# Kernel optimization log

Hardware: AMD Instinct MI355X
Metric: run time of the kernel (lower is better)

## Reference

```python
import jax, jax.numpy as jnp
import numpy as np

STRIDE = 2
IN_CH = 64
F_SCALE = 2
EMBED = 64  # int(in_ch * ss_exp_factor)


def _pixel_unshuffle(x, f):
    # out[b, (fi*f+fj)*c + cc, h, w] = x[b, cc, h*f+fi, w*f+fj]
    b, c, H, W = x.shape
    x = x.reshape(b, c, H // f, f, W // f, f)
    x = x.transpose(0, 3, 5, 1, 2, 4)  # b, fi, fj, c, h, w
    return x.reshape(b, f * f * c, H // f, W // f)


def _pixel_shuffle(x, f):
    b, fc, h, w = x.shape
    c = fc // (f * f)
    x = x.reshape(b, f, f, c, h, w)
    x = x.transpose(0, 3, 4, 1, 5, 2)  # b, c, h, fi, w, fj
    return x.reshape(b, c, h * f, w * f)


def _conv(x, w, b, dilation):
    out = jax.lax.conv_general_dilated(
        x, w, window_strides=(1, 1),
        padding=[(dilation, dilation), (dilation, dilation)],
        rhs_dilation=(dilation, dilation),
        dimension_numbers=('NCHW', 'OIHW', 'NCHW'))
    return out + b[None, :, None, None]


def _conv1x1(x, w, b):
    out = jax.lax.conv_general_dilated(
        x, w, window_strides=(1, 1), padding=[(0, 0), (0, 0)],
        dimension_numbers=('NCHW', 'OIHW', 'NCHW'))
    return out + b[None, :, None, None]


def _attention(x, wqk, f):
    b, c, H, W = x.shape
    # layer_norm over (c,h,w), no affine
    mu = jnp.mean(x, axis=(1, 2, 3), keepdims=True)
    var = jnp.var(x, axis=(1, 2, 3), keepdims=True)
    xx = (x - mu) / jnp.sqrt(var + 1e-5)
    ph, pw = (f - H % f) % f, (f - W % f) % f
    if ph or pw:
        xx = jnp.pad(xx, ((0, 0), (0, 0), (0, ph), (0, pw)))
        xv = jnp.pad(x, ((0, 0), (0, 0), (0, ph), (0, pw)))
    else:
        xv = x
    sh, sw = (H + ph) // f, (W + pw) // f
    B = b * f * f
    xu = _pixel_unshuffle(xx, f).reshape(B, c, sh, sw)
    vu = _pixel_unshuffle(xv, f).reshape(B, c, sh, sw)
    n = sh * sw
    qk = xu.transpose(0, 2, 3, 1).reshape(B, n, c)  # (B, n, c)
    v = vu.transpose(0, 2, 3, 1).reshape(B, n, c)
    q = qk @ wqk  # (B, n, e)
    q = q / jnp.maximum(jnp.linalg.norm(q, axis=-1, keepdims=True), 1e-12)
    attn = jnp.einsum('bne,bme->bnm', q, q) / jnp.sqrt(jnp.float32(wqk.shape[1]))
    attn = jax.nn.softmax(attn, axis=-1)
    out = jnp.einsum('bnm,bmc->bnc', attn, v)  # (B, n, c)
    out = out.reshape(B, sh, sw, c).transpose(0, 3, 1, 2)
    out = out.reshape(b, f * f * c, sh, sw)
    out = _pixel_shuffle(out, f)
    return out[:, :, :H, :W]


def setup_inputs() -> dict:
    key = jax.random.key(0)
    ks = jax.random.split(key, 8)
    c = IN_CH
    s3 = 1.0 / np.sqrt(c * 9)
    s1 = 1.0 / np.sqrt(c)
    return {
        'x': jax.random.normal(ks[0], (8, c, 128, 128), dtype=jnp.float32),
        'wqk': jax.random.normal(ks[1], (c, EMBED), dtype=jnp.float32) * np.sqrt(6.0 / (c + EMBED)),
        'conv1_w': jax.random.normal(ks[2], (c, c, 3, 3), dtype=jnp.float32) * s3,
        'conv1_b': jnp.zeros((c,), dtype=jnp.float32),
        'conv2_w': jax.random.normal(ks[3], (c, c, 3, 3), dtype=jnp.float32) * s3,
        'conv2_b': jnp.zeros((c,), dtype=jnp.float32),
        'conv3_w': jax.random.normal(ks[4], (c, c, 1, 1), dtype=jnp.float32) * s1,
        'conv3_b': jnp.zeros((c,), dtype=jnp.float32),
    }


def reference(x, wqk, conv1_w, conv1_b, conv2_w, conv2_b, conv3_w, conv3_b):
    f = F_SCALE * STRIDE
    a = x + _attention(x, wqk, f)
    y = jax.nn.relu(_conv(a, conv1_w, conv1_b, STRIDE))
    y = jax.nn.relu(_conv(y, conv2_w, conv2_b, STRIDE))
    y = _conv1x1(y, conv3_w, conv3_b)
    return x + y
```

## Files before the change

### kernel.cpp

```cpp
#include <hip/hip_runtime.h>

typedef unsigned short u16;
typedef unsigned int   u32;

typedef __attribute__((ext_vector_type(8))) short s16x8;
typedef __attribute__((ext_vector_type(4))) float f32x4;

__device__ __forceinline__ float bf2f(u16 u){
  union { u32 i; float f; } v; v.i = ((u32)u) << 16; return v.f;
}
__device__ __forceinline__ u16 f2bf(float f){
  union { float f; u32 i; } v; v.f = f;
  u32 x = v.i;
  return (u16)((x + 0x7fffu + ((x >> 16) & 1u)) >> 16);
}


__global__ __launch_bounds__(256) void k_lnstats(const float* __restrict__ x, float* __restrict__ stats){
  const int bb    = blockIdx.x >> 7;
  const int chunk = blockIdx.x & 127;
  const float4* p = (const float4*)(x + bb*1048576 + chunk*8192);
  float s = 0.f, ss = 0.f;
  #pragma unroll
  for (int i=0;i<8;++i){
    float4 v = p[threadIdx.x + (i<<8)];
    s  += v.x + v.y + v.z + v.w;
    ss += v.x*v.x + v.y*v.y + v.z*v.z + v.w*v.w;
  }
  #pragma unroll
  for (int off=32; off; off>>=1){ s += __shfl_down(s, off); ss += __shfl_down(ss, off); }
  __shared__ float rs[4], rss[4];
  const int lane = threadIdx.x & 63, wv = threadIdx.x >> 6;
  if (lane == 0){ rs[wv] = s; rss[wv] = ss; }
  __syncthreads();
  if (threadIdx.x == 0){
    atomicAdd(&stats[bb*2+0], rs[0]+rs[1]+rs[2]+rs[3]);
    atomicAdd(&stats[bb*2+1], rss[0]+rss[1]+rss[2]+rss[3]);
  }
}

__global__ __launch_bounds__(256) void k_wt(const float* __restrict__ w, u16* __restrict__ wt){
  int e = blockIdx.x*256 + threadIdx.x;
  int tap = e >> 12, co = (e >> 6) & 63, ci = e & 63;
  wt[e] = f2bf(w[(co*64 + ci)*9 + tap]);
}

__global__ __launch_bounds__(256) void k_qv(const float* __restrict__ x, const float* __restrict__ wqk,
                                            const float* __restrict__ stats,
                                            u16* __restrict__ qb, u16* __restrict__ vb){
  const int Bb = blockIdx.x >> 4;
  const int mt = blockIdx.x & 15;
  const int b = Bb >> 4, fi = (Bb >> 2) & 3, fj = Bb & 3;
  const float inv_n = 1.f/1048576.f;
  const float mu   = stats[2*b] * inv_n;
  const float var  = stats[2*b+1]*inv_n - mu*mu;
  const float rstd = rsqrtf(var + 1e-5f);

  __shared__ float xt[64][68];
  __shared__ float wk[64][68];
  __shared__ float red[64][17];
  const int t = threadIdx.x;
  const int m0 = mt << 6;

  #pragma unroll
  for (int i=0;i<16;++i){ int e = t+(i<<8); wk[e>>6][e&63] = wqk[e]; }
  #pragma unroll
  for (int i=0;i<16;++i){
    int e = t+(i<<8); int cc = e>>6, ml = e&63;
    int m = m0 + ml;
    int hh = ((m>>5)<<2)+fi, ww = ((m&31)<<2)+fj;
    xt[ml][cc] = (x[(((b<<6)+cc)<<14)+(hh<<7)+ww] - mu)*rstd;
  }
  __syncthreads();

  const int ty = t>>4, tx = t&15;
  float acc[4][4] = {};
  for (int cc=0; cc<64; ++cc){
    float a0=xt[(ty<<2)+0][cc], a1=xt[(ty<<2)+1][cc], a2=xt[(ty<<2)+2][cc], a3=xt[(ty<<2)+3][cc];
    float b0=wk[cc][(tx<<2)+0], b1=wk[cc][(tx<<2)+1], b2=wk[cc][(tx<<2)+2], b3=wk[cc][(tx<<2)+3];
    acc[0][0]+=a0*b0; acc[0][1]+=a0*b1; acc[0][2]+=a0*b2; acc[0][3]+=a0*b3;
    acc[1][0]+=a1*b0; acc[1][1]+=a1*b1; acc[1][2]+=a1*b2; acc[1][3]+=a1*b3;
    acc[2][0]+=a2*b0; acc[2][1]+=a2*b1; acc[2][2]+=a2*b2; acc[2][3]+=a2*b3;
    acc[3][0]+=a3*b0; acc[3][1]+=a3*b1; acc[3][2]+=a3*b2; acc[3][3]+=a3*b3;
  }
  #pragma unroll
  for (int i=0;i<4;++i){
    float pn = acc[i][0]*acc[i][0]+acc[i][1]*acc[i][1]+acc[i][2]*acc[i][2]+acc[i][3]*acc[i][3];
    red[(ty<<2)+i][tx] = pn;
  }
  __syncthreads();
  float inv[4];
  #pragma unroll
  for (int i=0;i<4;++i){
    float s = 0.f;
    #pragma unroll
    for (int k=0;k<16;++k) s += red[(ty<<2)+i][k];
    inv[i] = 1.f / fmaxf(sqrtf(s), 1e-12f);
  }
  #pragma unroll
  for (int i=0;i<4;++i)
    #pragma unroll
    for (int j=0;j<4;++j)
      xt[(ty<<2)+i][(tx<<2)+j] = acc[i][j]*inv[i];
  __syncthreads();
  #pragma unroll
  for (int i=0;i<16;++i){
    int e = t+(i<<8); int ml = e>>6, ee = e&63;
    qb[((Bb<<10)+m0+ml)*64 + ee] = f2bf(xt[ml][ee]);
  }
  #pragma unroll
  for (int i=0;i<16;++i){
    int e = t+(i<<8); int cc = e>>6, ml = e&63;
    int m = m0 + ml;
    int hh = ((m>>5)<<2)+fi, ww = ((m&31)<<2)+fj;
    wk[ml][cc] = x[(((b<<6)+cc)<<14)+(hh<<7)+ww];
  }
  __syncthreads();
  #pragma unroll
  for (int i=0;i<16;++i){
    int e = t+(i<<8); int cc = e>>6, ml = e&63;
    vb[(Bb<<16) + (cc<<10) + m0 + ml] = f2bf(wk[ml][cc]);
  }
}

__global__ __launch_bounds__(256) void k_attn(const u16* __restrict__ qb, const u16* __restrict__ vb,
                                              const float* __restrict__ x, u16* __restrict__ apad){
  const int Bb = blockIdx.x >> 4;
  const int qt = blockIdx.x & 15;
  const int b = Bb>>4, fi=(Bb>>2)&3, fj=Bb&3;
  __shared__ __align__(16) char lds[24576];
  const int KS = 0, VS = 8192, PS = 16384;

  const int t = threadIdx.x;
  const int w = t >> 6, lane = t & 63;
  const int lrow = lane & 15, lk = lane >> 4;

  const u16* qB = qb + (Bb<<16);
  const u16* vB = vb + (Bb<<16);

  const u16* qrp = qB + ((qt<<6) + (w<<4) + lrow)*64;
  const s16x8 qf0 = *(const s16x8*)(qrp + (lk<<3));
  const s16x8 qf1 = *(const s16x8*)(qrp + 32 + (lk<<3));

  f32x4 o_acc[4] = {};
  float lp[4] = {0.f,0.f,0.f,0.f};

  for (int kt=0; kt<16; ++kt){
    __syncthreads();
    #pragma unroll
    for (int c = t; c < 512; c += 256){
      int row = c >> 3, slot = c & 7;
      uint4 kv = *(const uint4*)(qB + ((kt<<6)+row)*64 + (slot<<3));
      *(uint4*)(lds + KS + row*128 + (((slot ^ (row&7)))<<4)) = kv;
      uint4 vv = *(const uint4*)(vB + (row<<10) + (kt<<6) + (slot<<3));
      *(uint4*)(lds + VS + row*128 + (((slot ^ (row&7)))<<4)) = vv;
    }
    __syncthreads();

    f32x4 s_acc[4] = {};
    #pragma unroll
    for (int nt=0; nt<4; ++nt){
      int key = (nt<<4) + lrow;
      const char* kb = lds + KS + key*128;
      s16x8 kf0 = *(const s16x8*)(kb + ((lk       ^ (key&7))<<4));
      s16x8 kf1 = *(const s16x8*)(kb + (((4+lk)   ^ (key&7))<<4));
      s_acc[nt] = __builtin_amdgcn_mfma_f32_16x16x32_bf16(qf0, kf0, s_acc[nt], 0,0,0);
      s_acc[nt] = __builtin_amdgcn_mfma_f32_16x16x32_bf16(qf1, kf1, s_acc[nt], 0,0,0);
    }

    #pragma unroll
    for (int nt=0; nt<4; ++nt)
      #pragma unroll
      for (int r=0; r<4; ++r){
        float p = __expf(s_acc[nt][r]*0.125f);
        lp[r] += p;
        int prow = (w<<4) + (lk<<2) + r;
        int key  = (nt<<4) + lrow;
        *(u16*)(lds + PS + prow*128 + ((key<<1) ^ ((prow&7)<<4))) = f2bf(p);
      }

    {
      int prow = (w<<4) + lrow;
      const char* pb = lds + PS + prow*128;
      s16x8 pf0 = *(const s16x8*)(pb + ((lk     ^ (prow&7))<<4));
      s16x8 pf1 = *(const s16x8*)(pb + (((4+lk) ^ (prow&7))<<4));
      #pragma unroll
      for (int nt=0; nt<4; ++nt){
        int ch = (nt<<4) + lrow;
        const char* vbp = lds + VS + ch*128;
        s16x8 vf0 = *(const s16x8*)(vbp + ((lk     ^ (ch&7))<<4));
        s16x8 vf1 = *(const s16x8*)(vbp + (((4+lk) ^ (ch&7))<<4));
        o_acc[nt] = __builtin_amdgcn_mfma_f32_16x16x32_bf16(pf0, vf0, o_acc[nt], 0,0,0);
        o_acc[nt] = __builtin_amdgcn_mfma_f32_16x16x32_bf16(pf1, vf1, o_acc[nt], 0,0,0);
      }
    }
  }

  #pragma unroll
  for (int r=0;r<4;++r){
    float s = lp[r];
    s += __shfl_xor(s, 1); s += __shfl_xor(s, 2);
    s += __shfl_xor(s, 4); s += __shfl_xor(s, 8);
    lp[r] = 1.f / s;
  }

  __syncthreads();
  float* os = (float*)lds;
  #pragma unroll
  for (int nt=0; nt<4; ++nt)
    #pragma unroll
    for (int r=0; r<4; ++r)
      os[((w<<4)+(lk<<2)+r)*68 + (nt<<4)+lrow] = o_acc[nt][r]*lp[r];
  __syncthreads();

  const int m0 = qt << 6;
  #pragma unroll
  for (int i=0;i<16;++i){
    int e = t+(i<<8);
    int cc = e>>6, ml = e&63;
    int m = m0 + ml;
    int hh = ((m>>5)<<2)+fi, ww = ((m&31)<<2)+fj;
    os[ml*68 + cc] += x[(((b<<6)+cc)<<14) + (hh<<7) + ww];
  }
  __syncthreads();
  #pragma unroll
  for (int i=0;i<16;++i){
    int e = t+(i<<8);
    int ml = e>>6, cc = e&63;
    int m = m0 + ml;
    int hh = ((m>>5)<<2)+fi, ww = ((m&31)<<2)+fj;
    apad[((b*132 + hh+2)*132 + ww+2)*64 + cc] = f2bf(os[ml*68 + cc]);
  }
}

__global__ __launch_bounds__(256) void k_conv3m(const u16* __restrict__ in, const u16* __restrict__ wt,
                                                const float* __restrict__ bias, u16* __restrict__ outp){
  const int seg = blockIdx.x;
  const int h   = blockIdx.y;
  const int b   = blockIdx.z;
  const int t = threadIdx.x;
  const int wv = t >> 6, lane = t & 63;
  const int lrow = lane & 15, lk = lane >> 4;
  const int co0 = wv << 4;
  const int w0 = seg << 6;

  s16x8 A[9][2];
  #pragma unroll
  for (int tap=0; tap<9; ++tap)
    #pragma unroll
    for (int hf=0; hf<2; ++hf)
      A[tap][hf] = *(const s16x8*)(wt + (((tap<<6) + co0 + lrow)<<6) + (hf<<5) + (lk<<3));

  float4 b4 = *(const float4*)&bias[co0 + (lk<<2)];
  f32x4 binit = {b4.x, b4.y, b4.z, b4.w};
  f32x4 acc[4] = {binit, binit, binit, binit};

  const int base_b = b * (132*132);
  #pragma unroll
  for (int dh=0; dh<3; ++dh){
    const u16* rowp = in + ((base_b + (h + (dh<<1))*132)<<6);
    #pragma unroll
    for (int dw=0; dw<3; ++dw){
      #pragma unroll
      for (int hf=0; hf<2; ++hf){
        #pragma unroll
        for (int pt=0; pt<4; ++pt){
          int wp = w0 + (pt<<4) + lrow + (dw<<1);
          s16x8 B = *(const s16x8*)(rowp + (wp<<6) + (hf<<5) + (lk<<3));
          acc[pt] = __builtin_amdgcn_mfma_f32_16x16x32_bf16(A[dh*3+dw][hf], B, acc[pt], 0,0,0);
        }
      }
    }
  }

  #pragma unroll
  for (int pt=0; pt<4; ++pt){
    int wp = w0 + (pt<<4) + lrow + 2;
    u16* op = outp + ((base_b + (h+2)*132 + wp)<<6) + co0 + (lk<<2);
    ushort4 o4;
    o4.x = f2bf(fmaxf(acc[pt][0], 0.f));
    o4.y = f2bf(fmaxf(acc[pt][1], 0.f));
    o4.z = f2bf(fmaxf(acc[pt][2], 0.f));
    o4.w = f2bf(fmaxf(acc[pt][3], 0.f));
    *(ushort4*)op = o4;
  }
}

__global__ __launch_bounds__(256) void k_conv1x1(const u16* __restrict__ y2, const float* __restrict__ w3,
                                                 const float* __restrict__ b3, const float* __restrict__ x,
                                                 float* __restrict__ out){
  const int b  = blockIdx.x >> 6;
  const int p0 = (blockIdx.x & 63) << 8;
  __shared__ u16  ys[256][68];
  __shared__ float w3s[64][68];
  __shared__ float bs[64];
  const int t = threadIdx.x;
  #pragma unroll
  for (int i=0;i<16;++i){ int e = t+(i<<8); w3s[e & 63][e >> 6] = w3[e]; }
  if (t < 64) bs[t] = b3[t];
  #pragma unroll
  for (int i=0;i<64;++i){
    int e = t + (i<<8);
    int px = e >> 6, ci = e & 63;
    int pg = p0 + px; int hh = pg >> 7, ww = pg & 127;
    ys[px][ci] = y2[((b*132 + hh+2)*132 + ww+2)*64 + ci];
  }
  __syncthreads();
  const int cog = (t >> 6) << 4;
  const int pl  = t & 63;
  float acc[16][4];
  #pragma unroll
  for (int c=0;c<16;++c){
    float bvv = bs[cog+c];
    acc[c][0]=bvv; acc[c][1]=bvv; acc[c][2]=bvv; acc[c][3]=bvv;
  }
  for (int c4=0;c4<64;c4+=4){
    float yv[4][4];
    #pragma unroll
    for (int p=0;p<4;++p){
      ushort4 u = *(const ushort4*)&ys[pl + (p<<6)][c4];
      yv[p][0]=bf2f(u.x); yv[p][1]=bf2f(u.y); yv[p][2]=bf2f(u.z); yv[p][3]=bf2f(u.w);
    }
    #pragma unroll
    for (int cq=0;cq<4;++cq){
      float4 w0 = *(const float4*)&w3s[c4+0][cog+(cq<<2)];
      float4 w1 = *(const float4*)&w3s[c4+1][cog+(cq<<2)];
      float4 w2 = *(const float4*)&w3s[c4+2][cog+(cq<<2)];
      float4 w3v = *(const float4*)&w3s[c4+3][cog+(cq<<2)];
      #pragma unroll
      for (int p=0;p<4;++p){
        acc[(cq<<2)+0][p] += yv[p][0]*w0.x + yv[p][1]*w1.x + yv[p][2]*w2.x + yv[p][3]*w3v.x;
        acc[(cq<<2)+1][p] += yv[p][0]*w0.y + yv[p][1]*w1.y + yv[p][2]*w2.y + yv[p][3]*w3v.y;
        acc[(cq<<2)+2][p] += yv[p][0]*w0.z + yv[p][1]*w1.z + yv[p][2]*w2.z + yv[p][3]*w3v.z;
        acc[(cq<<2)+3][p] += yv[p][0]*w0.w + yv[p][1]*w1.w + yv[p][2]*w2.w + yv[p][3]*w3v.w;
      }
    }
  }
  #pragma unroll
  for (int c=0;c<16;++c){
    int base = (((b<<6)+cog+c)<<14) + p0 + pl;
    #pragma unroll
    for (int p=0;p<4;++p){
      int gi = base + (p<<6);
      out[gi] = acc[c][p] + x[gi];
    }
  }
}

extern "C" void kernel_launch(void* const* d_in, const int* in_sizes, int n_in,
                              void* d_out, int out_size, void* d_ws, size_t ws_size,
                              hipStream_t stream){
  const float* x   = (const float*)d_in[0];
  const float* wqk = (const float*)d_in[1];
  const float* w1  = (const float*)d_in[2];
  const float* b1  = (const float*)d_in[3];
  const float* w2  = (const float*)d_in[4];
  const float* b2  = (const float*)d_in[5];
  const float* w3  = (const float*)d_in[6];
  const float* b3  = (const float*)d_in[7];
  float* out = (float*)d_out;

  float* stats = (float*)d_ws;
  u16* qb   = (u16*)((char*)d_ws + 256);
  u16* vb   = qb + 8388608;
  u16* apad = vb + 8388608;
  u16* y1   = qb;
  u16* y2   = apad;
  u16* wt1  = apad + 8921088;
  u16* wt2  = wt1 + 36864;

  hipMemsetAsync(stats, 0, 64, stream);
  k_wt<<<144, 256, 0, stream>>>(w1, wt1);
  k_wt<<<144, 256, 0, stream>>>(w2, wt2);
  k_lnstats<<<1024, 256, 0, stream>>>(x, stats);
  k_qv     <<<2048, 256, 0, stream>>>(x, wqk, stats, qb, vb);
  hipMemsetAsync(apad, 0, 17842176, stream);
  k_attn   <<<2048, 256, 0, stream>>>(qb, vb, x, apad);
  hipMemsetAsync(y1, 0, 17842176, stream);
  k_conv3m <<<dim3(2,128,8), 256, 0, stream>>>(apad, wt1, b1, y1);
  k_conv3m <<<dim3(2,128,8), 256, 0, stream>>>(y1, wt2, b2, y2);
  k_conv1x1<<<512, 256, 0, stream>>>(y2, w3, b3, x, out);
}
```

Before: 421.9 us.

## Process two query tiles per attention block and remap block order by batch

The attention kernel now handles two 64-row query tiles per block, so each K/V tile staged in LDS is reused twice and the block count halves. Block indices in both the attention and conv kernels are remapped so the batch index varies fastest, which spreads consecutive blocks across batches and likely changes how work lands on XCDs and L2. The cost is more registers per thread for the doubled accumulators and half as many attention blocks, which may reduce occupancy and parallelism.

```diff
diff --git a/kernel.cpp b/kernel.cpp
--- a/kernel.cpp
+++ b/kernel.cpp
@@ -125,9 +125,14 @@
 
 __global__ __launch_bounds__(256) void k_attn(const u16* __restrict__ qb, const u16* __restrict__ vb,
                                               const float* __restrict__ x, u16* __restrict__ apad){
-  const int Bb = blockIdx.x >> 4;
-  const int qt = blockIdx.x & 15;
-  const int b = Bb>>4, fi=(Bb>>2)&3, fj=Bb&3;
+  const int bid = blockIdx.x;
+  const int b   = bid & 7;
+  const int rem = bid >> 3;
+  const int qtp = rem >> 4;
+  const int sub = rem & 15;
+  const int Bb  = (b<<4) + sub;
+  const int fi = (sub>>2)&3, fj = sub&3;
+  const int qt0 = qtp << 1;
   __shared__ __align__(16) char lds[24576];
   const int KS = 0, VS = 8192, PS = 16384;
 
@@ -138,12 +143,16 @@
   const u16* qB = qb + (Bb<<16);
   const u16* vB = vb + (Bb<<16);
 
-  const u16* qrp = qB + ((qt<<6) + (w<<4) + lrow)*64;
-  const s16x8 qf0 = *(const s16x8*)(qrp + (lk<<3));
-  const s16x8 qf1 = *(const s16x8*)(qrp + 32 + (lk<<3));
-
-  f32x4 o_acc[4] = {};
-  float lp[4] = {0.f,0.f,0.f,0.f};
+  s16x8 qf[2][2];
+  #pragma unroll
+  for (int t2=0; t2<2; ++t2){
+    const u16* qrp = qB + (((qt0+t2)<<6) + (w<<4) + lrow)*64;
+    qf[t2][0] = *(const s16x8*)(qrp + (lk<<3));
+    qf[t2][1] = *(const s16x8*)(qrp + 32 + (lk<<3));
+  }
+
+  f32x4 o_acc[2][4] = {};
+  float lp[2][4] = {};
 
   for (int kt=0; kt<16; ++kt){
     __syncthreads();
@@ -157,87 +166,94 @@
     }
     __syncthreads();
 
-    f32x4 s_acc[4] = {};
-    #pragma unroll
-    for (int nt=0; nt<4; ++nt){
-      int key = (nt<<4) + lrow;
-      const char* kb = lds + KS + key*128;
-      s16x8 kf0 = *(const s16x8*)(kb + ((lk       ^ (key&7))<<4));
-      s16x8 kf1 = *(const s16x8*)(kb + (((4+lk)   ^ (key&7))<<4));
-      s_acc[nt] = __builtin_amdgcn_mfma_f32_16x16x32_bf16(qf0, kf0, s_acc[nt], 0,0,0);
-      s_acc[nt] = __builtin_amdgcn_mfma_f32_16x16x32_bf16(qf1, kf1, s_acc[nt], 0,0,0);
-    }
-
+    #pragma unroll
+    for (int t2=0; t2<2; ++t2){
+      f32x4 s_acc[4] = {};
+      #pragma unroll
+      for (int nt=0; nt<4; ++nt){
+        int key = (nt<<4) + lrow;
+        const char* kb = lds + KS + key*128;
+        s16x8 kf0 = *(const s16x8*)(kb + ((lk       ^ (key&7))<<4));
+        s16x8 kf1 = *(const s16x8*)(kb + (((4+lk)   ^ (key&7))<<4));
+        s_acc[nt] = __builtin_amdgcn_mfma_f32_16x16x32_bf16(qf[t2][0], kf0, s_acc[nt], 0,0,0);
+        s_acc[nt] = __builtin_amdgcn_mfma_f32_16x16x32_bf16(qf[t2][1], kf1, s_acc[nt], 0,0,0);
+      }
+      #pragma unroll
+      for (int nt=0; nt<4; ++nt)
+        #pragma unroll
+        for (int r=0; r<4; ++r){
+          float p = __expf(s_acc[nt][r]*0.125f);
+          lp[t2][r] += p;
+          int prow = (w<<4) + (lk<<2) + r;
+          int key  = (nt<<4) + lrow;
+          *(u16*)(lds + PS + prow*128 + ((key<<1) ^ ((prow&7)<<4))) = f2bf(p);
+        }
+      {
+        int prow = (w<<4) + lrow;
+        const char* pb = lds + PS + prow*128;
+        s16x8 pf0 = *(const s16x8*)(pb + ((lk     ^ (prow&7))<<4));
+        s16x8 pf1 = *(const s16x8*)(pb + (((4+lk) ^ (prow&7))<<4));
+        #pragma unroll
+        for (int nt=0; nt<4; ++nt){
+          int ch = (nt<<4) + lrow;
+          const char* vbp = lds + VS + ch*128;
+          s16x8 vf0 = *(const s16x8*)(vbp + ((lk     ^ (ch&7))<<4));
+          s16x8 vf1 = *(const s16x8*)(vbp + (((4+lk) ^ (ch&7))<<4));
+          o_acc[t2][nt] = __builtin_amdgcn_mfma_f32_16x16x32_bf16(pf0, vf0, o_acc[t2][nt], 0,0,0);
+          o_acc[t2][nt] = __builtin_amdgcn_mfma_f32_16x16x32_bf16(pf1, vf1, o_acc[t2][nt], 0,0,0);
+        }
+      }
+    }
+  }
+
+  #pragma unroll
+  for (int t2=0; t2<2; ++t2)
+    #pragma unroll
+    for (int r=0;r<4;++r){
+      float s = lp[t2][r];
+      s += __shfl_xor(s, 1); s += __shfl_xor(s, 2);
+      s += __shfl_xor(s, 4); s += __shfl_xor(s, 8);
+      lp[t2][r] = 1.f / s;
+    }
+
+  float* os = (float*)lds;
+  #pragma unroll
+  for (int t2=0; t2<2; ++t2){
+    __syncthreads();
     #pragma unroll
     for (int nt=0; nt<4; ++nt)
       #pragma unroll
-      for (int r=0; r<4; ++r){
-        float p = __expf(s_acc[nt][r]*0.125f);
-        lp[r] += p;
-        int prow = (w<<4) + (lk<<2) + r;
-        int key  = (nt<<4) + lrow;
-        *(u16*)(lds + PS + prow*128 + ((key<<1) ^ ((prow&7)<<4))) = f2bf(p);
-      }
-
-    {
-      int prow = (w<<4) + lrow;
-      const char* pb = lds + PS + prow*128;
-      s16x8 pf0 = *(const s16x8*)(pb + ((lk     ^ (prow&7))<<4));
-      s16x8 pf1 = *(const s16x8*)(pb + (((4+lk) ^ (prow&7))<<4));
-      #pragma unroll
-      for (int nt=0; nt<4; ++nt){
-        int ch = (nt<<4) + lrow;
-        const char* vbp = lds + VS + ch*128;
-        s16x8 vf0 = *(const s16x8*)(vbp + ((lk     ^ (ch&7))<<4));
-        s16x8 vf1 = *(const s16x8*)(vbp + (((4+lk) ^ (ch&7))<<4));
-        o_acc[nt] = __builtin_amdgcn_mfma_f32_16x16x32_bf16(pf0, vf0, o_acc[nt], 0,0,0);
-        o_acc[nt] = __builtin_amdgcn_mfma_f32_16x16x32_bf16(pf1, vf1, o_acc[nt], 0,0,0);
-      }
-    }
-  }
-
-  #pragma unroll
-  for (int r=0;r<4;++r){
-    float s = lp[r];
-    s += __shfl_xor(s, 1); s += __shfl_xor(s, 2);
-    s += __shfl_xor(s, 4); s += __shfl_xor(s, 8);
-    lp[r] = 1.f / s;
-  }
-
-  __syncthreads();
-  float* os = (float*)lds;
-  #pragma unroll
-  for (int nt=0; nt<4; ++nt)
-    #pragma unroll
-    for (int r=0; r<4; ++r)
-      os[((w<<4)+(lk<<2)+r)*68 + (nt<<4)+lrow] = o_acc[nt][r]*lp[r];
-  __syncthreads();
-
-  const int m0 = qt << 6;
-  #pragma unroll
-  for (int i=0;i<16;++i){
-    int e = t+(i<<8);
-    int cc = e>>6, ml = e&63;
-    int m = m0 + ml;
-    int hh = ((m>>5)<<2)+fi, ww = ((m&31)<<2)+fj;
-    os[ml*68 + cc] += x[(((b<<6)+cc)<<14) + (hh<<7) + ww];
-  }
-  __syncthreads();
-  #pragma unroll
-  for (int i=0;i<16;++i){
-    int e = t+(i<<8);
-    int ml = e>>6, cc = e&63;
-    int m = m0 + ml;
-    int hh = ((m>>5)<<2)+fi, ww = ((m&31)<<2)+fj;
-    apad[((b*132 + hh+2)*132 + ww+2)*64 + cc] = f2bf(os[ml*68 + cc]);
+      for (int r=0; r<4; ++r)
+        os[((w<<4)+(lk<<2)+r)*68 + (nt<<4)+lrow] = o_acc[t2][nt][r]*lp[t2][r];
+    __syncthreads();
+    const int m0 = (qt0+t2) << 6;
+    #pragma unroll
+    for (int i=0;i<16;++i){
+      int e = t+(i<<8);
+      int cc = e>>6, ml = e&63;
+      int m = m0 + ml;
+      int hh = ((m>>5)<<2)+fi, ww = ((m&31)<<2)+fj;
+      os[ml*68 + cc] += x[(((b<<6)+cc)<<14) + (hh<<7) + ww];
+    }
+    __syncthreads();
+    #pragma unroll
+    for (int i=0;i<16;++i){
+      int e = t+(i<<8);
+      int ml = e>>6, cc = e&63;
+      int m = m0 + ml;
+      int hh = ((m>>5)<<2)+fi, ww = ((m&31)<<2)+fj;
+      apad[((b*132 + hh+2)*132 + ww+2)*64 + cc] = f2bf(os[ml*68 + cc]);
+    }
   }
 }
 
 __global__ __launch_bounds__(256) void k_conv3m(const u16* __restrict__ in, const u16* __restrict__ wt,
                                                 const float* __restrict__ bias, u16* __restrict__ outp){
-  const int seg = blockIdx.x;
-  const int h   = blockIdx.y;
-  const int b   = blockIdx.z;
+  const int bid = blockIdx.x;
+  const int b   = bid & 7;
+  const int r   = bid >> 3;
+  const int h   = r & 127;
+  const int seg = r >> 7;
   const int t = threadIdx.x;
   const int wv = t >> 6, lane = t & 63;
   const int lrow = lane & 15, lk = lane >> 4;
@@ -375,9 +391,9 @@
   k_lnstats<<<1024, 256, 0, stream>>>(x, stats);
   k_qv     <<<2048, 256, 0, stream>>>(x, wqk, stats, qb, vb);
   hipMemsetAsync(apad, 0, 17842176, stream);
-  k_attn   <<<2048, 256, 0, stream>>>(qb, vb, x, apad);
+  k_attn   <<<1024, 256, 0, stream>>>(qb, vb, x, apad);
   hipMemsetAsync(y1, 0, 17842176, stream);
-  k_conv3m <<<dim3(2,128,8), 256, 0, stream>>>(apad, wt1, b1, y1);
-  k_conv3m <<<dim3(2,128,8), 256, 0, stream>>>(y1, wt2, b2, y2);
+  k_conv3m <<<2048, 256, 0, stream>>>(apad, wt1, b1, y1);
+  k_conv3m <<<2048, 256, 0, stream>>>(y1, wt2, b2, y2);
   k_conv1x1<<<512, 256, 0, stream>>>(y2, w3, b3, x, out);
 }
```

New measurement: 442.7 us. +4.9%, slower.
